# Kernel tuning notes

Hardware: AMD Instinct MI355X
Metric: run time of the kernel (lower is better)

The kernel has to match this reference:

```python
import jax, jax.numpy as jnp
import numpy as np

NEG_BIG = -9e15
ALPHA = 0.2  # LeakyReLU negative slope


def _gatm_layer(x, adj_mask, M, W, a_self, a_neighs):
    # x: [N, Fin], adj_mask: [N, N] bool, M: [N, N]
    h = x @ W                                   # [N, Fout]
    s = h @ a_self                              # [N, 1]
    n = h @ a_neighs                            # [N, 1]
    e = s + n.T                                 # [N, N] broadcast additive score
    e = jax.nn.leaky_relu(e * M, negative_slope=ALPHA)
    scores = jnp.where(adj_mask, e, NEG_BIG)
    attention = jax.nn.softmax(scores, axis=1)  # row-wise
    h_prime = attention @ h                     # [N, Fout]
    return jax.nn.elu(h_prime)                  # concat=True path


def setup_inputs() -> dict:
    key = jax.random.key(0)
    ks = jax.random.split(key, 8)
    N, D0, D1, D2 = 8192, 512, 256, 64
    scale = 0.05
    return {
        "x": jax.random.normal(ks[0], (N, D0), dtype=jnp.float32),
        "adj": jax.random.randint(ks[1], (N, N), 0, 2, dtype=jnp.int32),
        "M": jax.random.uniform(ks[2], (N, N), dtype=jnp.float32),
        "W0": jax.random.normal(ks[3], (D0, D1), dtype=jnp.float32) * scale,
        "a_self0": jax.random.normal(ks[4], (D1, 1), dtype=jnp.float32) * scale,
        "a_neighs0": jax.random.normal(ks[5], (D1, 1), dtype=jnp.float32) * scale,
        "W1": jax.random.normal(ks[6], (D1, D2), dtype=jnp.float32) * scale,
        "a_self1": jax.random.normal(ks[7], (D2, 1), dtype=jnp.float32) * scale,
        "a_neighs1": jax.random.normal(jax.random.fold_in(key, 99), (D2, 1), dtype=jnp.float32) * scale,
    }


def reference(x, adj, M, W0, a_self0, a_neighs0, W1, a_self1, a_neighs1):
    adj_mask = adj > 0
    x = _gatm_layer(x, adj_mask, M, W0, a_self0, a_neighs0)
    x = _gatm_layer(x, adj_mask, M, W1, a_self1, a_neighs1)
    return x
```

## Files before the change

### kernel.cpp

```cpp
#include <hip/hip_runtime.h>
#include <hip/hip_bf16.h>

constexpr int NN = 8192;
using uint = unsigned int;

typedef __bf16 bf16x8 __attribute__((ext_vector_type(8)));
typedef float f32x4 __attribute__((ext_vector_type(4)));
typedef float f32x16 __attribute__((ext_vector_type(16)));
typedef unsigned short ushort8_t __attribute__((ext_vector_type(8)));

__device__ __forceinline__ float eluf(float z) { return z > 0.f ? z : __expf(z) - 1.f; }

__device__ __forceinline__ unsigned short bf16_hi(float v) {
  unsigned u = __float_as_uint(v);
  unsigned r = u + 0x7fffu + ((u >> 16) & 1u);
  return (unsigned short)(r >> 16);
}
__device__ __forceinline__ float bf16_tof(unsigned short u) {
  return __uint_as_float(((unsigned)u) << 16);
}

__device__ __forceinline__ uint cvt_pk_bf16(float a, float b) {
  uint r;
  asm("v_cvt_pk_bf16_f32 %0, %1, %2" : "=v"(r) : "v"(a), "v"(b));
  return r;
}

__device__ __forceinline__ void lds_barrier() {
  asm volatile("s_waitcnt lgkmcnt(0)" ::: "memory");
  __builtin_amdgcn_s_barrier();
}

__global__ __launch_bounds__(256) void splitx_kernel(
    const float* __restrict__ X, unsigned short* __restrict__ Th,
    unsigned short* __restrict__ Tl) {
  const size_t tid = (size_t)blockIdx.x * 256 + threadIdx.x;
  const int kt = (int)(tid >> 13);
  const int row = (int)(tid & 8191);
  const float* src = X + (size_t)row * 512 + kt * 32;
  #pragma unroll
  for (int kc = 0; kc < 4; ++kc) {
    ushort8_t hi, lo;
    #pragma unroll
    for (int e = 0; e < 8; ++e) {
      const float v = src[kc * 8 + e];
      const unsigned short h = bf16_hi(v);
      hi[e] = h;
      lo[e] = bf16_hi(v - bf16_tof(h));
    }
    const size_t o = ((size_t)(kt * 4 + kc) * 8192 + row) * 8;
    *reinterpret_cast<ushort8_t*>(&Th[o]) = hi;
    *reinterpret_cast<ushort8_t*>(&Tl[o]) = lo;
  }
}

__global__ __launch_bounds__(256) void splitw_kernel(
    const float* __restrict__ W, unsigned short* __restrict__ Th,
    unsigned short* __restrict__ Tl) {
  const int tid = blockIdx.x * 256 + threadIdx.x;
  const int kb = tid >> 8;
  const int col = tid & 255;
  ushort8_t hi, lo;
  #pragma unroll
  for (int e = 0; e < 8; ++e) {
    const float v = W[(size_t)(kb * 8 + e) * 256 + col];
    const unsigned short h = bf16_hi(v);
    hi[e] = h;
    lo[e] = bf16_hi(v - bf16_tof(h));
  }
  const size_t o = ((size_t)kb * 256 + col) * 8;
  *reinterpret_cast<ushort8_t*>(&Th[o]) = hi;
  *reinterpret_cast<ushort8_t*>(&Tl[o]) = lo;
}

__global__ __launch_bounds__(512) void gemm1_mfma_kernel(
    const unsigned short* __restrict__ Axh, const unsigned short* __restrict__ Axl,
    const unsigned short* __restrict__ Bwh, const unsigned short* __restrict__ Bwl,
    float* __restrict__ C, unsigned short* __restrict__ Th,
    unsigned short* __restrict__ Tl) {
  const int t = threadIdx.x;
  const int lane = t & 63;
  const int cf = t >> 6;
  const int i0 = blockIdx.x * 32;
  const int col = cf * 32 + (lane & 31);
  const size_t abase = ((size_t)(lane >> 5) * 8192 + i0 + (lane & 31)) * 8;
  const size_t bbase = ((size_t)(lane >> 5) * 256 + col) * 8;

  f32x16 acc;
  #pragma unroll
  for (int i = 0; i < 16; ++i) acc[i] = 0.f;

  #pragma unroll 2
  for (int kt = 0; kt < 16; ++kt) {
    const size_t at = (size_t)kt * 4 * 8192 * 8;
    const size_t bt = (size_t)kt * 4 * 256 * 8;
    #pragma unroll
    for (int h = 0; h < 2; ++h) {
      const size_t ao = at + (size_t)h * 2 * 8192 * 8 + abase;
      const size_t bo = bt + (size_t)h * 2 * 256 * 8 + bbase;
      const bf16x8 ah = *reinterpret_cast<const bf16x8*>(Axh + ao);
      const bf16x8 al = *reinterpret_cast<const bf16x8*>(Axl + ao);
      const bf16x8 bh = *reinterpret_cast<const bf16x8*>(Bwh + bo);
      const bf16x8 bl = *reinterpret_cast<const bf16x8*>(Bwl + bo);
      acc = __builtin_amdgcn_mfma_f32_32x32x16_bf16(al, bh, acc, 0, 0, 0);
      acc = __builtin_amdgcn_mfma_f32_32x32x16_bf16(ah, bl, acc, 0, 0, 0);
      acc = __builtin_amdgcn_mfma_f32_32x32x16_bf16(ah, bh, acc, 0, 0, 0);
    }
  }

  #pragma unroll
  for (int reg = 0; reg < 16; ++reg) {
    const int row = (reg & 3) + 8 * (reg >> 2) + 4 * (lane >> 5);
    const float v = acc[reg];
    C[(size_t)(i0 + row) * 256 + col] = v;
    const unsigned short h = bf16_hi(v);
    const unsigned short l = bf16_hi(v - bf16_tof(h));
    const size_t o = ((size_t)(blockIdx.x * 4 + (row >> 3)) * 256 + col) * 8 + (row & 7);
    Th[o] = h;
    Tl[o] = l;
  }
}

template<int FOUT>
__global__ __launch_bounds__(256) void sn_kernel(
    const float* __restrict__ H, const float* __restrict__ a_self,
    const float* __restrict__ a_neigh, float* __restrict__ s, float* __restrict__ n) {
  const int wave = threadIdx.x >> 6;
  const int lane = threadIdx.x & 63;
  const int row = blockIdx.x * 4 + wave;
  float ds = 0.f, dn = 0.f;
  #pragma unroll
  for (int c = lane; c < FOUT; c += 64) {
    const float h = H[(size_t)row * FOUT + c];
    ds += h * a_self[c];
    dn += h * a_neigh[c];
  }
  #pragma unroll
  for (int off = 32; off > 0; off >>= 1) {
    ds += __shfl_down(ds, off);
    dn += __shfl_down(dn, off);
  }
  if (lane == 0) { s[row] = ds; n[row] = dn; }
}

__global__ __launch_bounds__(256) void mask_kernel(
    const int* __restrict__ adj, uint* __restrict__ Bm) {
  const size_t tg = (size_t)blockIdx.x * 256 + threadIdx.x;
  const int4 a = *reinterpret_cast<const int4*>(&adj[tg * 4]);
  uint nib = (a.x > 0 ? 1u : 0u) | (a.y > 0 ? 2u : 0u) |
             (a.z > 0 ? 4u : 0u) | (a.w > 0 ? 8u : 0u);
  const int lane = threadIdx.x & 63;
  uint v = nib << ((lane & 7) * 4);
  v |= __shfl_xor(v, 1);
  v |= __shfl_xor(v, 2);
  v |= __shfl_xor(v, 4);
  if ((lane & 7) == 0) Bm[tg >> 3] = v;
}

__global__ __launch_bounds__(256) void plsum_kernel(
    const float* __restrict__ pL, float* __restrict__ il) {
  const int i = blockIdx.x * 256 + threadIdx.x;
  il[i] = 1.0f / (pL[i] + pL[8192 + i]);
}

template<int F>
__global__ __launch_bounds__(256) void combine_kernel(
    const float* __restrict__ pO, const float* __restrict__ pL, float* __restrict__ out) {
  const size_t q = (size_t)blockIdx.x * 256 + threadIdx.x;
  const size_t base = q * 4;
  const int row = (int)(base / F);
  const float4 a = *reinterpret_cast<const float4*>(pO + base);
  const float4 b = *reinterpret_cast<const float4*>(pO + (size_t)8192 * F + base);
  const float il = 1.0f / (pL[row] + pL[8192 + row]);
  float4 o;
  o.x = eluf((a.x + b.x) * il);
  o.y = eluf((a.y + b.y) * il);
  o.z = eluf((a.z + b.z) * il);
  o.w = eluf((a.w + b.w) * il);
  *reinterpret_cast<float4*>(out + base) = o;
}

__global__ __launch_bounds__(256) void gemm2_fused_kernel(
    const float* __restrict__ pO1, const float* __restrict__ il1,
    const float* __restrict__ W, const float* __restrict__ a_self,
    const float* __restrict__ a_neigh, unsigned short* __restrict__ Th,
    unsigned short* __restrict__ Tl, float* __restrict__ s1,
    float* __restrict__ n1) {
  constexpr int K = 256, NOUT = 64, BM = 64, BK = 16;
  const size_t seg = (size_t)8192 * 256;
  __shared__ __align__(16) float As[BK][BM + 4];
  __shared__ __align__(16) float Ws[BK][NOUT];
  __shared__ float red_s[64][17];
  __shared__ float red_n[64][17];
  const int t = threadIdx.x;
  const int i0 = blockIdx.x * BM;
  const int tr = t >> 4;
  const int tc = t & 15;
  const int lr = t >> 2;
  const int lk = (t & 3) * 4;
  const int wk = t >> 4;
  const int wc = (t & 15) * 4;
  const float ilr = il1[i0 + lr];
  float acc[4][4] = {};
  for (int k0 = 0; k0 < K; k0 += BK) {
    const size_t aoff = (size_t)(i0 + lr) * 256 + k0 + lk;
    const float4 p0 = *reinterpret_cast<const float4*>(&pO1[aoff]);
    const float4 p1 = *reinterpret_cast<const float4*>(&pO1[seg + aoff]);
    As[lk + 0][lr] = eluf((p0.x + p1.x) * ilr);
    As[lk + 1][lr] = eluf((p0.y + p1.y) * ilr);
    As[lk + 2][lr] = eluf((p0.z + p1.z) * ilr);
    As[lk + 3][lr] = eluf((p0.w + p1.w) * ilr);
    *reinterpret_cast<float4*>(&Ws[wk][wc]) =
        *reinterpret_cast<const float4*>(&W[(size_t)(k0 + wk) * NOUT + wc]);
    __syncthreads();
    #pragma unroll
    for (int kk = 0; kk < BK; ++kk) {
      const float4 av = *reinterpret_cast<const float4*>(&As[kk][4 * tr]);
      const float4 wv = *reinterpret_cast<const float4*>(&Ws[kk][4 * tc]);
      const float a[4] = {av.x, av.y, av.z, av.w};
      const float w[4] = {wv.x, wv.y, wv.z, wv.w};
      #pragma unroll
      for (int i = 0; i < 4; ++i)
        #pragma unroll
        for (int j = 0; j < 4; ++j) acc[i][j] += a[i] * w[j];
    }
    __syncthreads();
  }
  float asv[4], anv[4];
  #pragma unroll
  for (int j = 0; j < 4; ++j) {
    asv[j] = a_self[4 * tc + j];
    anv[j] = a_neigh[4 * tc + j];
  }
  #pragma unroll
  for (int i = 0; i < 4; ++i) {
    float ps = 0.f, pn = 0.f;
    #pragma unroll
    for (int j = 0; j < 4; ++j) { ps += acc[i][j] * asv[j]; pn += acc[i][j] * anv[j]; }
    red_s[4 * tr + i][tc] = ps;
    red_n[4 * tr + i][tc] = pn;
  }
  #pragma unroll
  for (int i = 0; i < 4; ++i) {
    const int row = 4 * tr + i;
    const int tile = 2 * blockIdx.x + (row >> 5);
    const int kc = (row >> 3) & 3;
    const int e = row & 7;
    #pragma unroll
    for (int j = 0; j < 4; ++j) {
      const int col = 4 * tc + j;
      const float v = acc[i][j];
      const unsigned short h = bf16_hi(v);
      const unsigned short l = bf16_hi(v - bf16_tof(h));
      const size_t o = ((size_t)(tile * 4 + kc) * 64 + col) * 8 + e;
      Th[o] = h;
      Tl[o] = l;
    }
  }
  __syncthreads();
  if (t < 64) {
    float ss = 0.f, nn = 0.f;
    #pragma unroll
    for (int q = 0; q < 16; ++q) { ss += red_s[t][q]; nn += red_n[t][q]; }
    s1[i0 + t] = ss;
    n1[i0 + t] = nn;
  }
}

__global__ __launch_bounds__(1024, 4) void attn1_kernel(
    const float* __restrict__ Mm, const uint* __restrict__ Bm,
    const float* __restrict__ sv, const float* __restrict__ nv,
    const unsigned short* __restrict__ Th, const unsigned short* __restrict__ Tl,
    float* __restrict__ pO, float* __restrict__ pL) {
  constexpr int F = 256, NT = 4096 / 64;
  __shared__ __align__(16) uint Pa[2][2][2][8 * 132];
  __shared__ __align__(16) float nvs[8192];
  __shared__ float l_lds[64];

  const int t = threadIdx.x;
  const int lane = t & 63;
  const int w = t >> 6;
  const int cf = w & 7;
  const int ks = w >> 3;
  const int r = t >> 5;
  const int p2 = t & 31;
  const int i0 = blockIdx.x * 64;
  const int jh = blockIdx.y;
  const size_t jbase = (size_t)jh * 4096;
  const int jt = jh * 128;

  reinterpret_cast<float4*>(nvs)[t] = reinterpret_cast<const float4*>(nv + jbase)[t];

  const float svrA = sv[i0 + r];
  const float svrB = sv[i0 + 32 + r];
  const size_t mrowA = (size_t)(i0 + r) * NN + jbase;
  const size_t mrowB = mrowA + (size_t)32 * NN;
  const uint* mkrowA = Bm + (size_t)(i0 + r) * (NN / 32) + jh * 128;
  const uint* mkrowB = mkrowA + (size_t)32 * (NN / 32);
  const int col = cf * 32 + (lane & 31);
  const size_t bo0 = ((size_t)(lane >> 5) * F + col) * 8;
  const int pidx = (p2 >> 2) * 132 + r * 4 + (p2 & 3);
  const int aidx = (ks * 4 + (lane >> 5)) * 132 + (lane & 31) * 4;

  float2 MA_e = *reinterpret_cast<const float2*>(&Mm[mrowA + 2 * p2]);
  float2 MA_o = *reinterpret_cast<const float2*>(&Mm[mrowA + 64 + 2 * p2]);
  float2 MB_e = *reinterpret_cast<const float2*>(&Mm[mrowB + 2 * p2]);
  float2 MB_o = *reinterpret_cast<const float2*>(&Mm[mrowB + 64 + 2 * p2]);
  uint mkA_e = mkrowA[p2 >> 4];
  uint mkA_o = mkrowA[2 + (p2 >> 4)];
  uint mkB_e = mkrowB[p2 >> 4];
  uint mkB_o = mkrowB[2 + (p2 >> 4)];
  const size_t tb0 = (size_t)(jt + ks) * 8192;
  bf16x8 bh0_e = *reinterpret_cast<const bf16x8*>(Th + tb0 + bo0);
  bf16x8 bl0_e = *reinterpret_cast<const bf16x8*>(Tl + tb0 + bo0);
  bf16x8 bh1_e = *reinterpret_cast<const bf16x8*>(Th + tb0 + bo0 + 4096);
  bf16x8 bl1_e = *reinterpret_cast<const bf16x8*>(Tl + tb0 + bo0 + 4096);
  bf16x8 bh0_o, bl0_o, bh1_o, bl1_o;

  float rsumA = 0.f, rsumB = 0.f;
  f32x16 accA, accB;
  #pragma unroll
  for (int i = 0; i < 16; ++i) { accA[i] = 0.f; accB[i] = 0.f; }

  __syncthreads();

  float2 nv_e = *reinterpret_cast<const float2*>(&nvs[2 * p2]);
  float2 nv_o = *reinterpret_cast<const float2*>(&nvs[64 + 2 * p2]);

#define STEP1(TJ, MCA, MKA, MCB, MKB, NVC, BH0C, BL0C, BH1C, BL1C, BH0N, BL0N, BH1N, BL1N) \
  {                                                                               \
    const int t_j = (TJ);                                                         \
    const int jb = (t_j + 1 < NT) ? t_j + 1 : 0;                                  \
    const size_t tb = (size_t)(jt + 2 * jb + ks) * 8192;                          \
    BH0N = *reinterpret_cast<const bf16x8*>(Th + tb + bo0);                       \
    BL0N = *reinterpret_cast<const bf16x8*>(Tl + tb + bo0);                       \
    BH1N = *reinterpret_cast<const bf16x8*>(Th + tb + bo0 + 4096);                \
    BL1N = *reinterpret_cast<const bf16x8*>(Tl + tb + bo0 + 4096);                \
    float e0 = (svrA + NVC.x) * MCA.x; e0 = fmaxf(e0, 0.2f * e0); e0 = fminf(e0, 70.f); \
    float e1 = (svrA + NVC.y) * MCA.y; e1 = fmaxf(e1, 0.2f * e1); e1 = fminf(e1, 70.f); \
    float e2 = (svrB + NVC.x) * MCB.x; e2 = fmaxf(e2, 0.2f * e2); e2 = fminf(e2, 70.f); \
    float e3 = (svrB + NVC.y) * MCB.y; e3 = fmaxf(e3, 0.2f * e3); e3 = fminf(e3, 70.f); \
    const float pA0 = ((MKA >> (2 * (p2 & 15))) & 1u) ? __expf(e0) : 0.f;         \
    const float pA1 = ((MKA >> (2 * (p2 & 15) + 1)) & 1u) ? __expf(e1) : 0.f;     \
    const float pB0 = ((MKB >> (2 * (p2 & 15))) & 1u) ? __expf(e2) : 0.f;         \
    const float pB1 = ((MKB >> (2 * (p2 & 15) + 1)) & 1u) ? __expf(e3) : 0.f;     \
    rsumA += pA0 + pA1; rsumB += pB0 + pB1;                                       \
    const int jm = (t_j + 2 < NT) ? t_j + 2 : 0;                                  \
    MCA = *reinterpret_cast<const float2*>(&Mm[mrowA + (size_t)jm * 64 + 2 * p2]); \
    MKA = mkrowA[jm * 2 + (p2 >> 4)];                                             \
    MCB = *reinterpret_cast<const float2*>(&Mm[mrowB + (size_t)jm * 64 + 2 * p2]); \
    MKB = mkrowB[jm * 2 + (p2 >> 4)];                                             \
    NVC = *reinterpret_cast<const float2*>(&nvs[jm * 64 + 2 * p2]);               \
    const uint hwA = cvt_pk_bf16(pA0, pA1);                                       \
    const uint lwA = cvt_pk_bf16(pA0 - __uint_as_float(hwA << 16),                \
                                 pA1 - __uint_as_float(hwA & 0xffff0000u));       \
    const uint hwB = cvt_pk_bf16(pB0, pB1);                                       \
    const uint lwB = cvt_pk_bf16(pB0 - __uint_as_float(hwB << 16),                \
                                 pB1 - __uint_as_float(hwB & 0xffff0000u));       \
    Pa[t_j & 1][0][0][pidx] = hwA;                                                \
    Pa[t_j & 1][1][0][pidx] = lwA;                                                \
    Pa[t_j & 1][0][1][pidx] = hwB;                                                \
    Pa[t_j & 1][1][1][pidx] = lwB;                                                \
    lds_barrier();                                                                \
    const bf16x8 ahA0 = *reinterpret_cast<const bf16x8*>(&Pa[t_j & 1][0][0][aidx]);       \
    const bf16x8 alA0 = *reinterpret_cast<const bf16x8*>(&Pa[t_j & 1][1][0][aidx]);       \
    const bf16x8 ahA1 = *reinterpret_cast<const bf16x8*>(&Pa[t_j & 1][0][0][aidx + 264]); \
    const bf16x8 alA1 = *reinterpret_cast<const bf16x8*>(&Pa[t_j & 1][1][0][aidx + 264]); \
    const bf16x8 ahB0 = *reinterpret_cast<const bf16x8*>(&Pa[t_j & 1][0][1][aidx]);       \
    const bf16x8 alB0 = *reinterpret_cast<const bf16x8*>(&Pa[t_j & 1][1][1][aidx]);       \
    const bf16x8 ahB1 = *reinterpret_cast<const bf16x8*>(&Pa[t_j & 1][0][1][aidx + 264]); \
    const bf16x8 alB1 = *reinterpret_cast<const bf16x8*>(&Pa[t_j & 1][1][1][aidx + 264]); \
    accA = __builtin_amdgcn_mfma_f32_32x32x16_bf16(alA0, BH0C, accA, 0, 0, 0);    \
    accB = __builtin_amdgcn_mfma_f32_32x32x16_bf16(alB0, BH0C, accB, 0, 0, 0);    \
    accA = __builtin_amdgcn_mfma_f32_32x32x16_bf16(ahA0, BL0C, accA, 0, 0, 0);    \
    accB = __builtin_amdgcn_mfma_f32_32x32x16_bf16(ahB0, BL0C, accB, 0, 0, 0);    \
    accA = __builtin_amdgcn_mfma_f32_32x32x16_bf16(ahA0, BH0C, accA, 0, 0, 0);    \
    accB = __builtin_amdgcn_mfma_f32_32x32x16_bf16(ahB0, BH0C, accB, 0, 0, 0);    \
    accA = __builtin_amdgcn_mfma_f32_32x32x16_bf16(alA1, BH1C, accA, 0, 0, 0);    \
    accB = __builtin_amdgcn_mfma_f32_32x32x16_bf16(alB1, BH1C, accB, 0, 0, 0);    \
    accA = __builtin_amdgcn_mfma_f32_32x32x16_bf16(ahA1, BL1C, accA, 0, 0, 0);    \
    accB = __builtin_amdgcn_mfma_f32_32x32x16_bf16(ahB1, BL1C, accB, 0, 0, 0);    \
    accA = __builtin_amdgcn_mfma_f32_32x32x16_bf16(ahA1, BH1C, accA, 0, 0, 0);    \
    accB = __builtin_amdgcn_mfma_f32_32x32x16_bf16(ahB1, BH1C, accB, 0, 0, 0);    \
  }

  for (int tj = 0; tj < NT; tj += 2) {
    STEP1(tj,     MA_e, mkA_e, MB_e, mkB_e, nv_e, bh0_e, bl0_e, bh1_e, bl1_e, bh0_o, bl0_o, bh1_o, bl1_o)
    STEP1(tj + 1, MA_o, mkA_o, MB_o, mkB_o, nv_o, bh0_o, bl0_o, bh1_o, bl1_o, bh0_e, bl0_e, bh1_e, bl1_e)
  }
#undef STEP1

  #pragma unroll
  for (int off = 1; off < 32; off <<= 1) {
    rsumA += __shfl_xor(rsumA, off);
    rsumB += __shfl_xor(rsumB, off);
  }
  if (p2 == 0) { l_lds[r] = rsumA; l_lds[32 + r] = rsumB; }
  __syncthreads();
  if (t < 64) pL[(size_t)jh * 8192 + i0 + t] = l_lds[t];

  float* scratch = nvs;
  if (ks == 1) {
    #pragma unroll
    for (int reg = 0; reg < 16; ++reg) scratch[cf * 1024 + reg * 64 + lane] = accA[reg];
  }
  __syncthreads();
  if (ks == 0) {
    #pragma unroll
    for (int reg = 0; reg < 16; ++reg) {
      const int row = (reg & 3) + 8 * (reg >> 2) + 4 * (lane >> 5);
      pO[(size_t)jh * 8192 * F + (size_t)(i0 + row) * F + col] =
          accA[reg] + scratch[cf * 1024 + reg * 64 + lane];
    }
  }
  __syncthreads();
  if (ks == 1) {
    #pragma unroll
    for (int reg = 0; reg < 16; ++reg) scratch[cf * 1024 + reg * 64 + lane] = accB[reg];
  }
  __syncthreads();
  if (ks == 0) {
    #pragma unroll
    for (int reg = 0; reg < 16; ++reg) {
      const int row = (reg & 3) + 8 * (reg >> 2) + 4 * (lane >> 5);
      pO[(size_t)jh * 8192 * F + (size_t)(i0 + 32 + row) * F + col] =
          accB[reg] + scratch[cf * 1024 + reg * 64 + lane];
    }
  }
}

__global__ __launch_bounds__(1024, 4) void attn2_kernel(
    const float* __restrict__ Mm, const uint* __restrict__ Bm,
    const float* __restrict__ sv, const float* __restrict__ nv,
    const unsigned short* __restrict__ Th, const unsigned short* __restrict__ Tl,
    float* __restrict__ pO, float* __restrict__ pL) {
  constexpr int F = 64, NT = 4096 / 64;
  __shared__ __align__(16) uint Pa[2][2][2][8 * 132];
  __shared__ __align__(16) float nvs[4096];
  __shared__ float l_lds[64];

  const int t = threadIdx.x;
  const int lane = t & 63;
  const int w = t >> 6;
  const int rb = w & 1;
  const int cf = (w >> 1) & 3;
  const int ks = w >> 3;
  const int r = t >> 5;
  const int p2 = t & 31;
  const int i0 = blockIdx.x * 64;
  const int jh = blockIdx.y;
  const size_t jbase = (size_t)jh * 4096;
  const int jt = jh * 128;

  reinterpret_cast<float4*>(nvs)[t] = reinterpret_cast<const float4*>(nv + jbase)[t];

  const float svrA = sv[i0 + r];
  const float svrB = sv[i0 + 32 + r];
  const size_t mrowA = (size_t)(i0 + r) * NN + jbase;
  const size_t mrowB = mrowA + (size_t)32 * NN;
  const uint* mkrowA = Bm + (size_t)(i0 + r) * (NN / 32) + jh * 128;
  const uint* mkrowB = mkrowA + (size_t)32 * (NN / 32);
  const int col = cf * 16 + (lane & 15);
  const size_t bo2 = ((size_t)(lane >> 4) * F + col) * 8;
  const int pidx = (p2 >> 2) * 132 + r * 4 + (p2 & 3);
  const int aidx = (ks * 4 + (lane >> 4)) * 132 + (rb * 16 + (lane & 15)) * 4;

  float2 MA_e = *reinterpret_cast<const float2*>(&Mm[mrowA + 2 * p2]);
  float2 MA_o = *reinterpret_cast<const float2*>(&Mm[mrowA + 64 + 2 * p2]);
  float2 MB_e = *reinterpret_cast<const float2*>(&Mm[mrowB + 2 * p2]);
  float2 MB_o = *reinterpret_cast<const float2*>(&Mm[mrowB + 64 + 2 * p2]);
  uint mkA_e = mkrowA[p2 >> 4];
  uint mkA_o = mkrowA[2 + (p2 >> 4)];
  uint mkB_e = mkrowB[p2 >> 4];
  uint mkB_o = mkrowB[2 + (p2 >> 4)];
  const size_t tb0 = (size_t)(jt + ks) * 2048;
  bf16x8 bh_e = *reinterpret_cast<const bf16x8*>(Th + tb0 + bo2);
  bf16x8 bl_e = *reinterpret_cast<const bf16x8*>(Tl + tb0 + bo2);
  bf16x8 bh_o, bl_o;

  float rsumA = 0.f, rsumB = 0.f;
  f32x4 accA = {0.f, 0.f, 0.f, 0.f}, accA2 = {0.f, 0.f, 0.f, 0.f};
  f32x4 accB = {0.f, 0.f, 0.f, 0.f}, accB2 = {0.f, 0.f, 0.f, 0.f};

  __syncthreads();

  float2 nv_e = *reinterpret_cast<const float2*>(&nvs[2 * p2]);
  float2 nv_o = *reinterpret_cast<const float2*>(&nvs[64 + 2 * p2]);

#define STEP2(TJ, MCA, MKA, MCB, MKB, NVC, BHC, BLC, BHN, BLN)                    \
  {                                                                               \
    const int t_j = (TJ);                                                         \
    const int jb = (t_j + 1 < NT) ? t_j + 1 : 0;                                  \
    const size_t tb = (size_t)(jt + 2 * jb + ks) * 2048;                          \
    BHN = *reinterpret_cast<const bf16x8*>(Th + tb + bo2);                        \
    BLN = *reinterpret_cast<const bf16x8*>(Tl + tb + bo2);                        \
    float e0 = (svrA + NVC.x) * MCA.x; e0 = fmaxf(e0, 0.2f * e0); e0 = fminf(e0, 70.f); \
    float e1 = (svrA + NVC.y) * MCA.y; e1 = fmaxf(e1, 0.2f * e1); e1 = fminf(e1, 70.f); \
    float e2 = (svrB + NVC.x) * MCB.x; e2 = fmaxf(e2, 0.2f * e2); e2 = fminf(e2, 70.f); \
    float e3 = (svrB + NVC.y) * MCB.y; e3 = fmaxf(e3, 0.2f * e3); e3 = fminf(e3, 70.f); \
    const float pA0 = ((MKA >> (2 * (p2 & 15))) & 1u) ? __expf(e0) : 0.f;         \
    const float pA1 = ((MKA >> (2 * (p2 & 15) + 1)) & 1u) ? __expf(e1) : 0.f;     \
    const float pB0 = ((MKB >> (2 * (p2 & 15))) & 1u) ? __expf(e2) : 0.f;         \
    const float pB1 = ((MKB >> (2 * (p2 & 15) + 1)) & 1u) ? __expf(e3) : 0.f;     \
    rsumA += pA0 + pA1; rsumB += pB0 + pB1;                                       \
    const int jm = (t_j + 2 < NT) ? t_j + 2 : 0;                                  \
    MCA = *reinterpret_cast<const float2*>(&Mm[mrowA + (size_t)jm * 64 + 2 * p2]); \
    MKA = mkrowA[jm * 2 + (p2 >> 4)];                                             \
    MCB = *reinterpret_cast<const float2*>(&Mm[mrowB + (size_t)jm * 64 + 2 * p2]); \
    MKB = mkrowB[jm * 2 + (p2 >> 4)];                                             \
    NVC = *reinterpret_cast<const float2*>(&nvs[jm * 64 + 2 * p2]);               \
    const uint hwA = cvt_pk_bf16(pA0, pA1);                                       \
    const uint lwA = cvt_pk_bf16(pA0 - __uint_as_float(hwA << 16),                \
                                 pA1 - __uint_as_float(hwA & 0xffff0000u));       \
    const uint hwB = cvt_pk_bf16(pB0, pB1);                                       \
    const uint lwB = cvt_pk_bf16(pB0 - __uint_as_float(hwB << 16),                \
                                 pB1 - __uint_as_float(hwB & 0xffff0000u));       \
    Pa[t_j & 1][0][0][pidx] = hwA;                                                \
    Pa[t_j & 1][1][0][pidx] = lwA;                                                \
    Pa[t_j & 1][0][1][pidx] = hwB;                                                \
    Pa[t_j & 1][1][1][pidx] = lwB;                                                \
    lds_barrier();                                                                \
    const bf16x8 ahA = *reinterpret_cast<const bf16x8*>(&Pa[t_j & 1][0][0][aidx]); \
    const bf16x8 alA = *reinterpret_cast<const bf16x8*>(&Pa[t_j & 1][1][0][aidx]); \
    const bf16x8 ahB = *reinterpret_cast<const bf16x8*>(&Pa[t_j & 1][0][1][aidx]); \
    const bf16x8 alB = *reinterpret_cast<const bf16x8*>(&Pa[t_j & 1][1][1][aidx]); \
    accA  = __builtin_amdgcn_mfma_f32_16x16x32_bf16(alA, BHC, accA, 0, 0, 0);     \
    accB  = __builtin_amdgcn_mfma_f32_16x16x32_bf16(alB, BHC, accB, 0, 0, 0);     \
    accA2 = __builtin_amdgcn_mfma_f32_16x16x32_bf16(ahA, BLC, accA2, 0, 0, 0);    \
    accB2 = __builtin_amdgcn_mfma_f32_16x16x32_bf16(ahB, BLC, accB2, 0, 0, 0);    \
    accA  = __builtin_amdgcn_mfma_f32_16x16x32_bf16(ahA, BHC, accA, 0, 0, 0);     \
    accB  = __builtin_amdgcn_mfma_f32_16x16x32_bf16(ahB, BHC, accB, 0, 0, 0);     \
  }

  for (int tj = 0; tj < NT; tj += 2) {
    STEP2(tj,     MA_e, mkA_e, MB_e, mkB_e, nv_e, bh_e, bl_e, bh_o, bl_o)
    STEP2(tj + 1, MA_o, mkA_o, MB_o, mkB_o, nv_o, bh_o, bl_o, bh_e, bl_e)
  }
#undef STEP2

  #pragma unroll
  for (int off = 1; off < 32; off <<= 1) {
    rsumA += __shfl_xor(rsumA, off);
    rsumB += __shfl_xor(rsumB, off);
  }
  if (p2 == 0) { l_lds[r] = rsumA; l_lds[32 + r] = rsumB; }
  __syncthreads();
  if (t < 64) pL[(size_t)jh * 8192 + i0 + t] = l_lds[t];

  float* scratch = nvs;
  if (ks == 1) {
    #pragma unroll
    for (int reg = 0; reg < 4; ++reg)
      scratch[(w & 7) * 256 + reg * 64 + lane] = accA[reg] + accA2[reg];
  }
  __syncthreads();
  if (ks == 0) {
    #pragma unroll
    for (int reg = 0; reg < 4; ++reg) {
      const int row = rb * 16 + (lane >> 4) * 4 + reg;
      pO[(size_t)jh * 8192 * F + (size_t)(i0 + row) * F + col] =
          accA[reg] + accA2[reg] + scratch[(w & 7) * 256 + reg * 64 + lane];
    }
  }
  __syncthreads();
  if (ks == 1) {
    #pragma unroll
    for (int reg = 0; reg < 4; ++reg)
      scratch[(w & 7) * 256 + reg * 64 + lane] = accB[reg] + accB2[reg];
  }
  __syncthreads();
  if (ks == 0) {
    #pragma unroll
    for (int reg = 0; reg < 4; ++reg) {
      const int row = rb * 16 + (lane >> 4) * 4 + reg;
      pO[(size_t)jh * 8192 * F + (size_t)(i0 + 32 + row) * F + col] =
          accB[reg] + accB2[reg] + scratch[(w & 7) * 256 + reg * 64 + lane];
    }
  }
}

extern "C" void kernel_launch(void* const* d_in, const int* in_sizes, int n_in,
                              void* d_out, int out_size, void* d_ws, size_t ws_size,
                              hipStream_t stream) {
  const float* x   = (const float*)d_in[0];
  const int*   adj = (const int*)  d_in[1];
  const float* Mm  = (const float*)d_in[2];
  const float* W0  = (const float*)d_in[3];
  const float* as0 = (const float*)d_in[4];
  const float* an0 = (const float*)d_in[5];
  const float* W1  = (const float*)d_in[6];
  const float* as1 = (const float*)d_in[7];
  const float* an1 = (const float*)d_in[8];
  float* out = (float*)d_out;

  char* ws = (char*)d_ws;
  const size_t MB = 1048576;
  const size_t KB = 1024;
  float* h0  = (float*)(ws);
  uint*  Bm  = (uint*) (ws);
  unsigned short* Th0 = (unsigned short*)(ws + 18 * MB);
  unsigned short* Tl0 = (unsigned short*)(ws + 22 * MB);
  unsigned short* Th1 = (unsigned short*)(ws + 26 * MB);
  unsigned short* Tl1 = (unsigned short*)(ws + 27 * MB);
  float* s0  = (float*)(ws + 28 * MB);
  float* n0  = (float*)(ws + 28 * MB + 32 * KB);
  float* s1  = (float*)(ws + 28 * MB + 64 * KB);
  float* n1  = (float*)(ws + 28 * MB + 96 * KB);
  float* pL1 = (float*)(ws + 28 * MB + 128 * KB);
  float* pL2 = (float*)(ws + 28 * MB + 192 * KB);
  float* il1 = (float*)(ws + 28 * MB + 256 * KB);
  float* pO1 = (float*)(ws + 29 * MB);
  float* pO2 = (float*)(ws + 29 * MB);
  unsigned short* Txh = (unsigned short*)(ws + 64 * MB);
  unsigned short* Txl = (unsigned short*)(ws + 72 * MB);
  unsigned short* Twh = (unsigned short*)(ws + 80 * MB);
  unsigned short* Twl = (unsigned short*)(ws + 81 * MB);

  splitx_kernel<<<dim3(512), dim3(256), 0, stream>>>(x, Txh, Txl);
  splitw_kernel<<<dim3(64), dim3(256), 0, stream>>>(W0, Twh, Twl);
  gemm1_mfma_kernel<<<dim3(256), dim3(512), 0, stream>>>(Txh, Txl, Twh, Twl, h0, Th0, Tl0);
  sn_kernel<256><<<dim3(2048), dim3(256), 0, stream>>>(h0, as0, an0, s0, n0);
  mask_kernel<<<dim3(65536), dim3(256), 0, stream>>>(adj, Bm);
  attn1_kernel<<<dim3(128, 2), dim3(1024), 0, stream>>>(Mm, Bm, s0, n0, Th0, Tl0, pO1, pL1);
  plsum_kernel<<<dim3(32), dim3(256), 0, stream>>>(pL1, il1);
  gemm2_fused_kernel<<<dim3(128), dim3(256), 0, stream>>>(pO1, il1, W1, as1, an1,
                                                          Th1, Tl1, s1, n1);
  attn2_kernel<<<dim3(128, 2), dim3(1024), 0, stream>>>(Mm, Bm, s1, n1, Th1, Tl1, pO2, pL2);
  combine_kernel<64><<<dim3(512), dim3(256), 0, stream>>>(pO2, pL2, out);
}
```

Measured before the change: 325.0 us.

## Fuse adjacency bitmask packing into first attention kernel

Removes the standalone mask_kernel and has attn1 read the int32 adjacency matrix directly, using it for masking and packing it into the bitmask that attn2 consumes. This saves one launch and a separate full pass over the 256MB adjacency array. In exchange, attn1 now loads 8 bytes per element pair instead of a packed bit, and adds shuffles and scattered stores to its inner loop, so the loop may become more memory-bound.

```diff
diff --git a/kernel.cpp b/kernel.cpp
--- a/kernel.cpp
+++ b/kernel.cpp
@@ -141,20 +141,6 @@
     dn += __shfl_down(dn, off);
   }
   if (lane == 0) { s[row] = ds; n[row] = dn; }
-}
-
-__global__ __launch_bounds__(256) void mask_kernel(
-    const int* __restrict__ adj, uint* __restrict__ Bm) {
-  const size_t tg = (size_t)blockIdx.x * 256 + threadIdx.x;
-  const int4 a = *reinterpret_cast<const int4*>(&adj[tg * 4]);
-  uint nib = (a.x > 0 ? 1u : 0u) | (a.y > 0 ? 2u : 0u) |
-             (a.z > 0 ? 4u : 0u) | (a.w > 0 ? 8u : 0u);
-  const int lane = threadIdx.x & 63;
-  uint v = nib << ((lane & 7) * 4);
-  v |= __shfl_xor(v, 1);
-  v |= __shfl_xor(v, 2);
-  v |= __shfl_xor(v, 4);
-  if ((lane & 7) == 0) Bm[tg >> 3] = v;
 }
 
 __global__ __launch_bounds__(256) void plsum_kernel(
@@ -268,10 +254,10 @@
 }
 
 __global__ __launch_bounds__(1024, 4) void attn1_kernel(
-    const float* __restrict__ Mm, const uint* __restrict__ Bm,
+    const float* __restrict__ Mm, const int* __restrict__ adj,
     const float* __restrict__ sv, const float* __restrict__ nv,
     const unsigned short* __restrict__ Th, const unsigned short* __restrict__ Tl,
-    float* __restrict__ pO, float* __restrict__ pL) {
+    float* __restrict__ pO, float* __restrict__ pL, uint* __restrict__ BmOut) {
   constexpr int F = 256, NT = 4096 / 64;
   __shared__ __align__(16) uint Pa[2][2][2][8 * 132];
   __shared__ __align__(16) float nvs[8192];
@@ -295,21 +281,20 @@
   const float svrB = sv[i0 + 32 + r];
   const size_t mrowA = (size_t)(i0 + r) * NN + jbase;
   const size_t mrowB = mrowA + (size_t)32 * NN;
-  const uint* mkrowA = Bm + (size_t)(i0 + r) * (NN / 32) + jh * 128;
-  const uint* mkrowB = mkrowA + (size_t)32 * (NN / 32);
+  const size_t bmrowA = (size_t)(i0 + r) * (NN / 32) + jh * 128;
+  const size_t bmrowB = bmrowA + (size_t)32 * (NN / 32);
   const int col = cf * 32 + (lane & 31);
   const size_t bo0 = ((size_t)(lane >> 5) * F + col) * 8;
   const int pidx = (p2 >> 2) * 132 + r * 4 + (p2 & 3);
   const int aidx = (ks * 4 + (lane >> 5)) * 132 + (lane & 31) * 4;
+  const int mshift = 2 * (p2 & 15);
 
   float2 MA_e = *reinterpret_cast<const float2*>(&Mm[mrowA + 2 * p2]);
   float2 MA_o = *reinterpret_cast<const float2*>(&Mm[mrowA + 64 + 2 * p2]);
   float2 MB_e = *reinterpret_cast<const float2*>(&Mm[mrowB + 2 * p2]);
   float2 MB_o = *reinterpret_cast<const float2*>(&Mm[mrowB + 64 + 2 * p2]);
-  uint mkA_e = mkrowA[p2 >> 4];
-  uint mkA_o = mkrowA[2 + (p2 >> 4)];
-  uint mkB_e = mkrowB[p2 >> 4];
-  uint mkB_o = mkrowB[2 + (p2 >> 4)];
+  int2 aA = *reinterpret_cast<const int2*>(&adj[mrowA + 2 * p2]);
+  int2 aB = *reinterpret_cast<const int2*>(&adj[mrowB + 2 * p2]);
   const size_t tb0 = (size_t)(jt + ks) * 8192;
   bf16x8 bh0_e = *reinterpret_cast<const bf16x8*>(Th + tb0 + bo0);
   bf16x8 bl0_e = *reinterpret_cast<const bf16x8*>(Tl + tb0 + bo0);
@@ -327,7 +312,7 @@
   float2 nv_e = *reinterpret_cast<const float2*>(&nvs[2 * p2]);
   float2 nv_o = *reinterpret_cast<const float2*>(&nvs[64 + 2 * p2]);
 
-#define STEP1(TJ, MCA, MKA, MCB, MKB, NVC, BH0C, BL0C, BH1C, BL1C, BH0N, BL0N, BH1N, BL1N) \
+#define STEP1(TJ, MCA, MCB, NVC, BH0C, BL0C, BH1C, BL1C, BH0N, BL0N, BH1N, BL1N)  \
   {                                                                               \
     const int t_j = (TJ);                                                         \
     const int jb = (t_j + 1 < NT) ? t_j + 1 : 0;                                  \
@@ -340,16 +325,28 @@
     float e1 = (svrA + NVC.y) * MCA.y; e1 = fmaxf(e1, 0.2f * e1); e1 = fminf(e1, 70.f); \
     float e2 = (svrB + NVC.x) * MCB.x; e2 = fmaxf(e2, 0.2f * e2); e2 = fminf(e2, 70.f); \
     float e3 = (svrB + NVC.y) * MCB.y; e3 = fmaxf(e3, 0.2f * e3); e3 = fminf(e3, 70.f); \
-    const float pA0 = ((MKA >> (2 * (p2 & 15))) & 1u) ? __expf(e0) : 0.f;         \
-    const float pA1 = ((MKA >> (2 * (p2 & 15) + 1)) & 1u) ? __expf(e1) : 0.f;     \
-    const float pB0 = ((MKB >> (2 * (p2 & 15))) & 1u) ? __expf(e2) : 0.f;         \
-    const float pB1 = ((MKB >> (2 * (p2 & 15) + 1)) & 1u) ? __expf(e3) : 0.f;     \
+    const float pA0 = (aA.x > 0) ? __expf(e0) : 0.f;                              \
+    const float pA1 = (aA.y > 0) ? __expf(e1) : 0.f;                              \
+    const float pB0 = (aB.x > 0) ? __expf(e2) : 0.f;                              \
+    const float pB1 = (aB.y > 0) ? __expf(e3) : 0.f;                              \
+                \
+    uint wA = ((aA.x > 0 ? 1u : 0u) | (aA.y > 0 ? 2u : 0u)) << mshift;            \
+    uint wB = ((aB.x > 0 ? 1u : 0u) | (aB.y > 0 ? 2u : 0u)) << mshift;            \
+    wA |= __shfl_xor(wA, 1); wB |= __shfl_xor(wB, 1);                             \
+    wA |= __shfl_xor(wA, 2); wB |= __shfl_xor(wB, 2);                             \
+    wA |= __shfl_xor(wA, 4); wB |= __shfl_xor(wB, 4);                             \
+    wA |= __shfl_xor(wA, 8); wB |= __shfl_xor(wB, 8);                             \
+    if ((p2 & 15) == 0) {                                                         \
+      BmOut[bmrowA + t_j * 2 + (p2 >> 4)] = wA;                                   \
+      BmOut[bmrowB + t_j * 2 + (p2 >> 4)] = wB;                                   \
+    }                                                                             \
     rsumA += pA0 + pA1; rsumB += pB0 + pB1;                                       \
     const int jm = (t_j + 2 < NT) ? t_j + 2 : 0;                                  \
+    const int jm1 = (t_j + 1 < NT) ? t_j + 1 : 0;                                 \
     MCA = *reinterpret_cast<const float2*>(&Mm[mrowA + (size_t)jm * 64 + 2 * p2]); \
-    MKA = mkrowA[jm * 2 + (p2 >> 4)];                                             \
     MCB = *reinterpret_cast<const float2*>(&Mm[mrowB + (size_t)jm * 64 + 2 * p2]); \
-    MKB = mkrowB[jm * 2 + (p2 >> 4)];                                             \
+    aA = *reinterpret_cast<const int2*>(&adj[mrowA + (size_t)jm1 * 64 + 2 * p2]); \
+    aB = *reinterpret_cast<const int2*>(&adj[mrowB + (size_t)jm1 * 64 + 2 * p2]); \
     NVC = *reinterpret_cast<const float2*>(&nvs[jm * 64 + 2 * p2]);               \
     const uint hwA = cvt_pk_bf16(pA0, pA1);                                       \
     const uint lwA = cvt_pk_bf16(pA0 - __uint_as_float(hwA << 16),                \
@@ -385,8 +382,8 @@
   }
 
   for (int tj = 0; tj < NT; tj += 2) {
-    STEP1(tj,     MA_e, mkA_e, MB_e, mkB_e, nv_e, bh0_e, bl0_e, bh1_e, bl1_e, bh0_o, bl0_o, bh1_o, bl1_o)
-    STEP1(tj + 1, MA_o, mkA_o, MB_o, mkB_o, nv_o, bh0_o, bl0_o, bh1_o, bl1_o, bh0_e, bl0_e, bh1_e, bl1_e)
+    STEP1(tj,     MA_e, MB_e, nv_e, bh0_e, bl0_e, bh1_e, bl1_e, bh0_o, bl0_o, bh1_o, bl1_o)
+    STEP1(tj + 1, MA_o, MB_o, nv_o, bh0_o, bl0_o, bh1_o, bl1_o, bh0_e, bl0_e, bh1_e, bl1_e)
   }
 #undef STEP1
 
@@ -620,8 +617,8 @@
   splitw_kernel<<<dim3(64), dim3(256), 0, stream>>>(W0, Twh, Twl);
   gemm1_mfma_kernel<<<dim3(256), dim3(512), 0, stream>>>(Txh, Txl, Twh, Twl, h0, Th0, Tl0);
   sn_kernel<256><<<dim3(2048), dim3(256), 0, stream>>>(h0, as0, an0, s0, n0);
-  mask_kernel<<<dim3(65536), dim3(256), 0, stream>>>(adj, Bm);
-  attn1_kernel<<<dim3(128, 2), dim3(1024), 0, stream>>>(Mm, Bm, s0, n0, Th0, Tl0, pO1, pL1);
+  attn1_kernel<<<dim3(128, 2), dim3(1024), 0, stream>>>(Mm, adj, s0, n0, Th0, Tl0,
+                                                        pO1, pL1, Bm);
   plsum_kernel<<<dim3(32), dim3(256), 0, stream>>>(pL1, il1);
   gemm2_fused_kernel<<<dim3(128), dim3(256), 0, stream>>>(pO1, il1, W1, as1, an1,
                                                           Th1, Tl1, s1, n1);
```

Measured after the change: 362.8 us. +11.6%, slower.
